# Optimization experiments

Hardware: AMD Instinct MI355X
Metric: run time of the kernel (lower is better)

The kernel has to match this reference:

```python
import jax, jax.numpy as jnp
import numpy as np

NORM_EPS = 1e-5
NUM_HEAD = 16
DIM_HEAD = 32
DIM_HIDDEN = 512
DIM_POS = 2
N, S = 4, 8192


def setup_inputs() -> dict:
    key = jax.random.key(0)
    ks = jax.random.split(key, 16)
    d = DIM_HIDDEN
    inp = {
        "Q": jax.random.normal(ks[0], (N, S, d), jnp.float32),
        "K": jax.random.normal(ks[1], (N, S, d), jnp.float32),
        "V": jax.random.normal(ks[2], (N, S, d), jnp.float32),
        "position": jax.random.uniform(ks[3], (N, S, DIM_POS), jnp.float32),
        "W_Q": jax.random.normal(ks[4], (d, d), jnp.float32) * (1.0 / np.sqrt(d)),
        "W_K": jax.random.normal(ks[5], (d, d), jnp.float32) * (1.0 / np.sqrt(d)),
        "W_V": jax.random.normal(ks[6], (d, d), jnp.float32) * (1.0 / np.sqrt(d)),
        "b_Q": jnp.zeros((d,), jnp.float32),
        "b_K": jnp.zeros((d,), jnp.float32),
        "b_V": jnp.zeros((d,), jnp.float32),
        "ln_w_K": jnp.ones((NUM_HEAD, DIM_HEAD), jnp.float32),
        "ln_b_K": jnp.zeros((NUM_HEAD, DIM_HEAD), jnp.float32),
        "ln_w_V": jnp.ones((NUM_HEAD, DIM_HEAD), jnp.float32),
        "ln_b_V": jnp.zeros((NUM_HEAD, DIM_HEAD), jnp.float32),
        # torch Linear(dim_hidden + dim_position*num_head, dim_hidden): weight [out, in]
        "fc_W": jax.random.normal(ks[7], (d, d + DIM_POS * NUM_HEAD), jnp.float32) * (1.0 / np.sqrt(d + DIM_POS * NUM_HEAD)),
        "fc_b": jnp.zeros((d,), jnp.float32),
    }
    return inp


def _proj_heads(x, W, b):
    # [N,S,D] @ [D,D] + [D] -> [N,H,S,Dh]
    n, s, d = x.shape
    y = x @ W + b
    return y.reshape(n, s, NUM_HEAD, DIM_HEAD).transpose(0, 2, 1, 3)


def _ln(x, w, b):
    # per-head layernorm over last dim; w,b: [H,Dh] broadcast as [1,H,1,Dh]
    mu = jnp.mean(x, axis=-1, keepdims=True)
    var = jnp.mean((x - mu) ** 2, axis=-1, keepdims=True)
    xn = (x - mu) * jax.lax.rsqrt(var + NORM_EPS)
    return xn * w[None, :, None, :] + b[None, :, None, :]


def reference(Q, K, V, position, W_Q, W_K, W_V, b_Q, b_K, b_V,
              ln_w_K, ln_b_K, ln_w_V, ln_b_V, fc_W, fc_b):
    n, s, d = Q.shape
    q = _proj_heads(Q, W_Q, b_Q)                    # [N,H,S,Dh]
    k = _ln(_proj_heads(K, W_K, b_K), ln_w_K, ln_b_K)
    v = _ln(_proj_heads(V, W_V, b_V), ln_w_V, ln_b_V)
    pos = jnp.broadcast_to(position[:, None, :, :], (n, NUM_HEAD, s, DIM_POS))
    q = jnp.concatenate([pos, q], axis=-1)          # [N,H,S,P+Dh]
    k = jnp.concatenate([pos, k], axis=-1)
    v = jnp.concatenate([pos, v], axis=-1)
    # Galerkin linear attention: Q @ (K^T V / seqlen), no softmax
    ktv = jnp.einsum('nhsd,nhse->nhde', k, v) / s   # [N,H,P+Dh,P+Dh]
    x = jnp.einsum('nhsd,nhde->nhse', q, ktv)       # [N,H,S,P+Dh]
    x = x.transpose(0, 2, 1, 3).reshape(n, s, NUM_HEAD * (DIM_POS + DIM_HEAD))
    return x @ fc_W.T + fc_b
```

## Files before the change

### kernel.cpp

```cpp
#include <hip/hip_runtime.h>
#include <hip/hip_bf16.h>

typedef short short8 __attribute__((ext_vector_type(8)));
typedef float f32x4 __attribute__((ext_vector_type(4)));
typedef unsigned int uint4v __attribute__((ext_vector_type(4)));

__device__ __forceinline__ short f2bf(float f) {
  unsigned u = __builtin_bit_cast(unsigned, f);
  u += 0x7fffu + ((u >> 16) & 1u);
  return (short)(u >> 16);
}
__device__ __forceinline__ float bf2f(short s) {
  unsigned u = ((unsigned)(unsigned short)s) << 16;
  return __builtin_bit_cast(float, u);
}
__device__ __forceinline__ unsigned pk2(float a, float b) {
  __hip_bfloat162 h = __float22bfloat162_rn(float2{a, b});
  unsigned u;
  __builtin_memcpy(&u, &h, 4);
  return u;
}
__device__ __forceinline__ void gl_lds16(const void* g, void* l) {
  __builtin_amdgcn_global_load_lds(
      (const __attribute__((address_space(1))) unsigned int*)g,
      (__attribute__((address_space(3))) unsigned int*)l, 16, 0, 0);
}

__global__ __launch_bounds__(256) void wt_kernel(
    const float* __restrict__ WK, const float* __restrict__ WV,
    short* __restrict__ Wt)
{
  const int z = blockIdx.z;
  const float* W = (z == 0) ? WK : WV;
  short* o = Wt + (size_t)z * 512 * 512;
  __shared__ short t[64][65];
  const int k0 = blockIdx.y * 64, n0 = blockIdx.x * 64;
  const int c = threadIdx.x & 63, rb = threadIdx.x >> 6;
#pragma unroll
  for (int p = 0; p < 16; ++p) {
    const int kk = p * 4 + rb;
    t[kk][c] = f2bf(W[(size_t)(k0 + kk) * 512 + n0 + c]);
  }
  __syncthreads();
#pragma unroll
  for (int p = 0; p < 16; ++p) {
    const int nn = p * 4 + rb;
    o[(size_t)(n0 + nn) * 512 + k0 + c] = t[c][nn];
  }
}

__global__ __launch_bounds__(512) void proj_kernel(
    const float* __restrict__ Kin, const float* __restrict__ Vin,
    const short* __restrict__ Wt,
    const float* __restrict__ bK, const float* __restrict__ bV,
    short* __restrict__ kp, short* __restrict__ vp)
{
  const int phys = blockIdx.x;
  const int log_ = (phys & 7) * 64 + (phys >> 3);
  const int z = log_ >> 8;
  const int rem = log_ & 255;
  const int row0 = (rem >> 1) * 256;
  const int col0 = (rem & 1) * 256;

  const float* X    = (z == 0) ? Kin : Vin;
  const float* bias = (z == 0) ? bK  : bV;
  const short* Wz   = Wt + (size_t)z * 512 * 512;
  short* dst        = (z == 0) ? kp : vp;

  __shared__ short a_lds[2][256 * 32];
  __shared__ short b_lds[2][256 * 32];

  const int tid = threadIdx.x;
  const int lane = tid & 63, wv = tid >> 6;
  const int wr = wv >> 2, wc = wv & 3;
  const int fr = lane & 15, fg = lane >> 4;

  f32x4 acc[8][4];
#pragma unroll
  for (int i = 0; i < 8; ++i)
#pragma unroll
    for (int j = 0; j < 4; ++j) acc[i][j] = (f32x4){0.f, 0.f, 0.f, 0.f};

  const int ar = tid >> 1;
  const int ak = (tid & 1) * 16;
  const int bl8 = lane * 8;

  {
#pragma unroll
    for (int i = 0; i < 2; ++i) {
      const int nb = i * 128 + wv * 16;
      gl_lds16(Wz + (size_t)(col0 + nb + (lane >> 2)) * 512 + (lane & 3) * 8,
               &b_lds[0][nb * 32 + bl8]);
    }
    const f32x4* ap = (const f32x4*)(X + (size_t)(row0 + ar) * 512 + ak);
    f32x4 f0 = ap[0], f1 = ap[1], f2 = ap[2], f3 = ap[3];
    uint4v s0, s1;
    s0[0] = pk2(f0[0], f0[1]); s0[1] = pk2(f0[2], f0[3]);
    s0[2] = pk2(f1[0], f1[1]); s0[3] = pk2(f1[2], f1[3]);
    s1[0] = pk2(f2[0], f2[1]); s1[1] = pk2(f2[2], f2[3]);
    s1[2] = pk2(f3[0], f3[1]); s1[3] = pk2(f3[2], f3[3]);
    *(uint4v*)&a_lds[0][ar * 32 + ak] = s0;
    *(uint4v*)&a_lds[0][ar * 32 + ak + 8] = s1;
  }
  __syncthreads();

  for (int t = 0; t < 16; ++t) {
    const int cur = t & 1;
    const bool pf = (t < 15);
    f32x4 p0, p1, p2, p3;
    if (pf) {
      const int k1 = (t + 1) * 32;
      short* bn = b_lds[cur ^ 1];
#pragma unroll
      for (int i = 0; i < 2; ++i) {
        const int nb = i * 128 + wv * 16;
        gl_lds16(Wz + (size_t)(col0 + nb + (lane >> 2)) * 512 + k1 + (lane & 3) * 8,
                 &bn[nb * 32 + bl8]);
      }
      const f32x4* ap = (const f32x4*)(X + (size_t)(row0 + ar) * 512 + k1 + ak);
      p0 = ap[0]; p1 = ap[1]; p2 = ap[2]; p3 = ap[3];
    }

    const short* acur = a_lds[cur];
    const short* bcur = b_lds[cur];
    short8 af[8], bfr[4];
#pragma unroll
    for (int mi = 0; mi < 8; ++mi)
      af[mi] = *(const short8*)&acur[(wr * 128 + mi * 16 + fr) * 32 + fg * 8];
#pragma unroll
    for (int ni = 0; ni < 4; ++ni)
      bfr[ni] = *(const short8*)&bcur[(wc * 64 + ni * 16 + fr) * 32 + fg * 8];
#pragma unroll
    for (int mi = 0; mi < 8; ++mi)
#pragma unroll
      for (int ni = 0; ni < 4; ++ni)
        acc[mi][ni] = __builtin_amdgcn_mfma_f32_16x16x32_bf16(af[mi], bfr[ni], acc[mi][ni], 0, 0, 0);

    if (pf) {
      short* an = a_lds[cur ^ 1];
      uint4v s0, s1;
      s0[0] = pk2(p0[0], p0[1]); s0[1] = pk2(p0[2], p0[3]);
      s0[2] = pk2(p1[0], p1[1]); s0[3] = pk2(p1[2], p1[3]);
      s1[0] = pk2(p2[0], p2[1]); s1[1] = pk2(p2[2], p2[3]);
      s1[2] = pk2(p3[0], p3[1]); s1[3] = pk2(p3[2], p3[3]);
      *(uint4v*)&an[ar * 32 + ak] = s0;
      *(uint4v*)&an[ar * 32 + ak + 8] = s1;
    }
    __syncthreads();
  }

#pragma unroll
  for (int ni = 0; ni < 4; ++ni) {
    const int gc = col0 + wc * 64 + ni * 16 + fr;
    const float bv = bias[gc];
#pragma unroll
    for (int mi = 0; mi < 8; ++mi) {
#pragma unroll
      for (int r = 0; r < 4; ++r) {
        const int gr = row0 + wr * 128 + mi * 16 + fg * 4 + r;
        dst[(size_t)gr * 512 + gc] = f2bf(acc[mi][ni][r] + bv);
      }
    }
  }
}

#define SC 256
#define TP 264

__global__ __launch_bounds__(256) void ktv_kernel(
    const short* __restrict__ kp, const short* __restrict__ vp,
    const float* __restrict__ pos,
    const float* __restrict__ lnwK, const float* __restrict__ lnbK,
    const float* __restrict__ lnwV, const float* __restrict__ lnbV,
    float* __restrict__ ktv)
{
  const int nh = blockIdx.y;
  const int n = nh >> 4, h = nh & 15;
  const int s0 = blockIdx.x * SC;
  const int tid = threadIdx.x;

  __shared__ short klds[48 * TP];
  __shared__ short vlds[48 * TP];
  __shared__ float lw[2][32], lb[2][32];

  if (tid < 32) {
    lw[0][tid] = lnwK[h * 32 + tid]; lb[0][tid] = lnbK[h * 32 + tid];
    lw[1][tid] = lnwV[h * 32 + tid]; lb[1][tid] = lnbV[h * 32 + tid];
  }
  __syncthreads();

  const size_t rowix = (size_t)n * 8192 + (s0 + tid);
  {
    const short8* src = (const short8*)(kp + rowix * 512 + h * 32);
    short8 r0 = src[0], r1 = src[1], r2 = src[2], r3 = src[3];
// ... 48 lines not shown
    for (int i = 0; i < 3; ++i) acc[i] = (f32x4){0.f, 0.f, 0.f, 0.f};
    for (int kk = 0; kk < SC; kk += 32) {
      short8 a = *(const short8*)&klds[(wv * 16 + fr) * TP + kk + fg * 8];
#pragma unroll
      for (int ni = 0; ni < 3; ++ni) {
        short8 b = *(const short8*)&vlds[(ni * 16 + fr) * TP + kk + fg * 8];
        acc[ni] = __builtin_amdgcn_mfma_f32_16x16x32_bf16(a, b, acc[ni], 0, 0, 0);
      }
    }
#pragma unroll
    for (int ni = 0; ni < 3; ++ni) {
      const int ei = ni * 16 + fr;
      if (ei < 34) {
        const int er = (ei < 32) ? ei + 2 : ei - 32;
#pragma unroll
        for (int r = 0; r < 4; ++r) {
          const int di = wv * 16 + fg * 4 + r;
          if (di < 34) {
            const int dr = (di < 32) ? di + 2 : di - 32;
            atomicAdd(&ktv[((size_t)nh * 34 + dr) * 34 + er], acc[ni][r]);
          }
        }
      }
    }
  }
}

__global__ __launch_bounds__(256) void sbuild_kernel(
    const float* __restrict__ ktv, const float* __restrict__ fcW,
    const float* __restrict__ bQ, float* __restrict__ St, float* __restrict__ Pp3)
{
  const int nh = blockIdx.x;
  const int n = nh >> 4, h = nh & 15;
  __shared__ float g[34 * 34];
  __shared__ float bq[32];
  for (int i = threadIdx.x; i < 34 * 34; i += 256)
    g[i] = ktv[(size_t)nh * 34 * 34 + i] * (1.f / 8192.f);
  if (threadIdx.x < 32) bq[threadIdx.x] = bQ[h * 32 + threadIdx.x];
  __syncthreads();

  for (int o = threadIdx.x; o < 512; o += 256) {
    float wcol[34];
#pragma unroll
    for (int e = 0; e < 34; ++e) wcol[e] = fcW[(size_t)o * 544 + h * 34 + e];
    float p0 = 0.f, p1 = 0.f;
#pragma unroll
    for (int e = 0; e < 34; ++e) { p0 += g[e] * wcol[e]; p1 += g[34 + e] * wcol[e]; }
    float rv = 0.f;
    float* srow = St + ((size_t)n * 512 + o) * 512 + h * 32;
#pragma unroll
    for (int j = 0; j < 32; ++j) {
      float s = 0.f;
#pragma unroll
      for (int e = 0; e < 34; ++e) s += g[(j + 2) * 34 + e] * wcol[e];
      srow[j] = s;
      rv += bq[j] * s;
    }
    atomicAdd(&Pp3[((size_t)n * 3 + 0) * 512 + o], p0);
    atomicAdd(&Pp3[((size_t)n * 3 + 1) * 512 + o], p1);
    atomicAdd(&Pp3[((size_t)n * 3 + 2) * 512 + o], rv);
  }
}

__global__ __launch_bounds__(256) void cbuild_kernel(
    const float* __restrict__ St, const float* __restrict__ WQ,
    short* __restrict__ Ct)
{
  const int n = blockIdx.z;
  const int row0 = blockIdx.y * 128;
  const int col0 = blockIdx.x * 128;
  const float* A = St + (size_t)n * 512 * 512;
  const float* B = WQ;

  __shared__ short a_lds[128 * 32];
  __shared__ short b_lds[128 * 32];

  const int tid = threadIdx.x;
  const int lane = tid & 63, wv = tid >> 6;
  const int wr = wv >> 1, wc = wv & 1;
  const int fr = lane & 15, fg = lane >> 4;
  const int ar = tid >> 1, ak = (tid & 1) * 16;

  f32x4 acc[4][4];
#pragma unroll
  for (int i = 0; i < 4; ++i)
#pragma unroll
    for (int j = 0; j < 4; ++j) acc[i][j] = (f32x4){0.f, 0.f, 0.f, 0.f};

  for (int k0 = 0; k0 < 512; k0 += 32) {
    __syncthreads();
    {
      const f32x4* ap = (const f32x4*)(A + (size_t)(row0 + ar) * 512 + k0 + ak);
      f32x4 f0 = ap[0], f1 = ap[1], f2 = ap[2], f3 = ap[3];
      uint4v s0, s1;
      s0[0] = pk2(f0[0], f0[1]); s0[1] = pk2(f0[2], f0[3]);
      s0[2] = pk2(f1[0], f1[1]); s0[3] = pk2(f1[2], f1[3]);
      s1[0] = pk2(f2[0], f2[1]); s1[1] = pk2(f2[2], f2[3]);
      s1[2] = pk2(f3[0], f3[1]); s1[3] = pk2(f3[2], f3[3]);
      *(uint4v*)&a_lds[ar * 32 + ak] = s0;
      *(uint4v*)&a_lds[ar * 32 + ak + 8] = s1;
      const f32x4* bp = (const f32x4*)(B + (size_t)(col0 + ar) * 512 + k0 + ak);
      f32x4 g0 = bp[0], g1 = bp[1], g2 = bp[2], g3 = bp[3];
      s0[0] = pk2(g0[0], g0[1]); s0[1] = pk2(g0[2], g0[3]);
      s0[2] = pk2(g1[0], g1[1]); s0[3] = pk2(g1[2], g1[3]);
      s1[0] = pk2(g2[0], g2[1]); s1[1] = pk2(g2[2], g2[3]);
      s1[2] = pk2(g3[0], g3[1]); s1[3] = pk2(g3[2], g3[3]);
      *(uint4v*)&b_lds[ar * 32 + ak] = s0;
      *(uint4v*)&b_lds[ar * 32 + ak + 8] = s1;
    }
    __syncthreads();

    short8 af[4], bfr[4];
#pragma unroll
    for (int mi = 0; mi < 4; ++mi)
      af[mi] = *(const short8*)&a_lds[(wr * 64 + mi * 16 + fr) * 32 + fg * 8];
#pragma unroll
    for (int ni = 0; ni < 4; ++ni)
      bfr[ni] = *(const short8*)&b_lds[(wc * 64 + ni * 16 + fr) * 32 + fg * 8];
#pragma unroll
    for (int mi = 0; mi < 4; ++mi)
#pragma unroll
      for (int ni = 0; ni < 4; ++ni)
        acc[mi][ni] = __builtin_amdgcn_mfma_f32_16x16x32_bf16(af[mi], bfr[ni], acc[mi][ni], 0, 0, 0);
  }

#pragma unroll
  for (int ni = 0; ni < 4; ++ni) {
    const int gc = col0 + wc * 64 + ni * 16 + fr;
#pragma unroll
    for (int mi = 0; mi < 4; ++mi)
#pragma unroll
      for (int r = 0; r < 4; ++r) {
        const int gr = row0 + wr * 64 + mi * 16 + fg * 4 + r;
        Ct[((size_t)n * 512 + gr) * 512 + gc] = f2bf(acc[mi][ni][r]);
      }
  }
}

__global__ __launch_bounds__(512) void fuse_kernel(
    const float* __restrict__ Q, const short* __restrict__ Ct,
    const float* __restrict__ pos, const float* __restrict__ Pp3,
    const float* __restrict__ fcb, float* __restrict__ out)
{
  const int phys = blockIdx.x;
  const int log_ = (phys & 7) * 32 + (phys >> 3);
  const int n = log_ >> 6;
  const int rem = log_ & 63;
  const int row0 = (rem >> 1) * 256;
  const int col0 = (rem & 1) * 256;

  const float* X = Q + (size_t)n * 8192 * 512;
  const short* B = Ct + (size_t)n * 512 * 512;

  __shared__ short a_lds[2][256 * 32];
  __shared__ short b_lds[2][256 * 32];

  const int tid = threadIdx.x;
  const int lane = tid & 63, wv = tid >> 6;
  const int wr = wv >> 2, wc = wv & 3;
  const int fr = lane & 15, fg = lane >> 4;

  f32x4 acc[8][4];
#pragma unroll
  for (int i = 0; i < 8; ++i)
#pragma unroll
    for (int j = 0; j < 4; ++j) acc[i][j] = (f32x4){0.f, 0.f, 0.f, 0.f};

  const int ar = tid >> 1;
  const int ak = (tid & 1) * 16;
  const int bl8 = lane * 8;

  {
#pragma unroll
    for (int i = 0; i < 2; ++i) {
      const int nb = i * 128 + wv * 16;
      gl_lds16(B + (size_t)(col0 + nb + (lane >> 2)) * 512 + (lane & 3) * 8,
               &b_lds[0][nb * 32 + bl8]);
    }
    const f32x4* ap = (const f32x4*)(X + (size_t)(row0 + ar) * 512 + ak);
    f32x4 f0 = ap[0], f1 = ap[1], f2 = ap[2], f3 = ap[3];
    uint4v s0, s1;
    s0[0] = pk2(f0[0], f0[1]); s0[1] = pk2(f0[2], f0[3]);
    s0[2] = pk2(f1[0], f1[1]); s0[3] = pk2(f1[2], f1[3]);
    s1[0] = pk2(f2[0], f2[1]); s1[1] = pk2(f2[2], f2[3]);
    s1[2] = pk2(f3[0], f3[1]); s1[3] = pk2(f3[2], f3[3]);
    *(uint4v*)&a_lds[0][ar * 32 + ak] = s0;
    *(uint4v*)&a_lds[0][ar * 32 + ak + 8] = s1;
  }
  __syncthreads();

  for (int t = 0; t < 16; ++t) {
    const int cur = t & 1;
    const bool pf = (t < 15);
    f32x4 p0, p1, p2, p3;
    if (pf) {
      const int k1 = (t + 1) * 32;
      short* bn = b_lds[cur ^ 1];
#pragma unroll
      for (int i = 0; i < 2; ++i) {
        const int nb = i * 128 + wv * 16;
        gl_lds16(B + (size_t)(col0 + nb + (lane >> 2)) * 512 + k1 + (lane & 3) * 8,
                 &bn[nb * 32 + bl8]);
      }
      const f32x4* ap = (const f32x4*)(X + (size_t)(row0 + ar) * 512 + k1 + ak);
      p0 = ap[0]; p1 = ap[1]; p2 = ap[2]; p3 = ap[3];
    }

    const short* acur = a_lds[cur];
    const short* bcur = b_lds[cur];
    short8 af[8], bfr[4];
#pragma unroll
    for (int mi = 0; mi < 8; ++mi)
      af[mi] = *(const short8*)&acur[(wr * 128 + mi * 16 + fr) * 32 + fg * 8];
#pragma unroll
    for (int ni = 0; ni < 4; ++ni)
      bfr[ni] = *(const short8*)&bcur[(wc * 64 + ni * 16 + fr) * 32 + fg * 8];
#pragma unroll
    for (int mi = 0; mi < 8; ++mi)
#pragma unroll
      for (int ni = 0; ni < 4; ++ni)
        acc[mi][ni] = __builtin_amdgcn_mfma_f32_16x16x32_bf16(af[mi], bfr[ni], acc[mi][ni], 0, 0, 0);

    if (pf) {
      short* an = a_lds[cur ^ 1];
      uint4v s0, s1;
      s0[0] = pk2(p0[0], p0[1]); s0[1] = pk2(p0[2], p0[3]);
      s0[2] = pk2(p1[0], p1[1]); s0[3] = pk2(p1[2], p1[3]);
      s1[0] = pk2(p2[0], p2[1]); s1[1] = pk2(p2[2], p2[3]);
      s1[2] = pk2(p3[0], p3[1]); s1[3] = pk2(p3[2], p3[3]);
      *(uint4v*)&an[ar * 32 + ak] = s0;
      *(uint4v*)&an[ar * 32 + ak + 8] = s1;
    }
    __syncthreads();
  }

  float pp0[4], pp1[4], rv[4];
#pragma unroll
  for (int ni = 0; ni < 4; ++ni) {
    const int gc = col0 + wc * 64 + ni * 16 + fr;
    pp0[ni] = Pp3[((size_t)n * 3 + 0) * 512 + gc];
    pp1[ni] = Pp3[((size_t)n * 3 + 1) * 512 + gc];
    rv[ni]  = Pp3[((size_t)n * 3 + 2) * 512 + gc] + fcb[gc];
  }
#pragma unroll
  for (int mi = 0; mi < 8; ++mi) {
#pragma unroll
    for (int r = 0; r < 4; ++r) {
      const int gr = row0 + wr * 128 + mi * 16 + fg * 4 + r;
      const float* pr = pos + ((size_t)n * 8192 + gr) * 2;
      const float q0 = pr[0], q1 = pr[1];
#pragma unroll
      for (int ni = 0; ni < 4; ++ni) {
        const int gc = col0 + wc * 64 + ni * 16 + fr;
        out[((size_t)n * 8192 + gr) * 512 + gc] =
            acc[mi][ni][r] + pp0[ni] * q0 + pp1[ni] * q1 + rv[ni];
      }
    }
  }
}

extern "C" void kernel_launch(void* const* d_in, const int* in_sizes, int n_in,
                              void* d_out, int out_size, void* d_ws, size_t ws_size,
                              hipStream_t stream) {
  const float* Q    = (const float*)d_in[0];
  const float* Kin  = (const float*)d_in[1];
  const float* Vin  = (const float*)d_in[2];
  const float* pos  = (const float*)d_in[3];
  const float* WQ   = (const float*)d_in[4];
  const float* WK   = (const float*)d_in[5];
  const float* WV   = (const float*)d_in[6];
  const float* bQ   = (const float*)d_in[7];
  const float* bK   = (const float*)d_in[8];
  const float* bV   = (const float*)d_in[9];
  const float* lnwK = (const float*)d_in[10];
  const float* lnbK = (const float*)d_in[11];
  const float* lnwV = (const float*)d_in[12];
  const float* lnbV = (const float*)d_in[13];
  const float* fcW  = (const float*)d_in[14];
  const float* fcb  = (const float*)d_in[15];

  char* ws = (char*)d_ws;
  const size_t KP_B  = (size_t)4 * 8192 * 512 * 2;
  const size_t KTV_B = (size_t)64 * 34 * 34 * 4;
  const size_t ST_B  = (size_t)4 * 512 * 512 * 4;
  const size_t CT_B  = (size_t)4 * 512 * 512 * 2;
  const size_t WT_B  = (size_t)2 * 512 * 512 * 2;
  const size_t PP_B  = (size_t)4 * 3 * 512 * 4;
  short* kp  = (short*)ws;
  short* vp  = (short*)(ws + KP_B);
  float* ktv = (float*)(ws + 2 * KP_B);
  float* St  = (float*)(ws + 2 * KP_B + KTV_B);
  short* Ct  = (short*)(ws + 2 * KP_B + KTV_B + ST_B);
  short* Wt  = (short*)(ws + 2 * KP_B + KTV_B + ST_B + CT_B);
  float* Pp3 = (float*)(ws + 2 * KP_B + KTV_B + ST_B + CT_B + WT_B);

  (void)hipMemsetAsync(ktv, 0, KTV_B, stream);
  (void)hipMemsetAsync(Pp3, 0, PP_B, stream);
  hipLaunchKernelGGL(wt_kernel, dim3(8, 8, 2), dim3(256), 0, stream, WK, WV, Wt);
  hipLaunchKernelGGL(proj_kernel, dim3(512), dim3(512), 0, stream,
                     Kin, Vin, Wt, bK, bV, kp, vp);
  hipLaunchKernelGGL(ktv_kernel, dim3(32, 64), dim3(256), 0, stream,
                     kp, vp, pos, lnwK, lnbK, lnwV, lnbV, ktv);
  hipLaunchKernelGGL(sbuild_kernel, dim3(64), dim3(256), 0, stream,
                     ktv, fcW, bQ, St, Pp3);
  hipLaunchKernelGGL(cbuild_kernel, dim3(4, 4, 4), dim3(256), 0, stream,
                     St, WQ, Ct);
  hipLaunchKernelGGL(fuse_kernel, dim3(256), dim3(512), 0, stream,
                     Q, Ct, pos, Pp3, fcb, (float*)d_out);
}
```

Before: 231.7 us.

## Deepen K tile to 64 with swizzled LDS and manual waitcnt pipelining in GEMMs

Both projection and fused output GEMM kernels now load 64-wide K tiles into XOR-swizzled LDS buffers. This halves loop iterations and barriers and aims to remove LDS bank conflicts on fragment reads. Synchronisation is replaced with explicit vmcnt/lgkmcnt waits, a single raw barrier, and elevated priority around MFMA bursts. The change doubles LDS use per block, which may limit occupancy despite the added launch-bounds hint.

```diff
diff --git a/kernel.cpp b/kernel.cpp
--- a/kernel.cpp
+++ b/kernel.cpp
@@ -49,7 +49,7 @@
   }
 }
 
-__global__ __launch_bounds__(512) void proj_kernel(
+__global__ __launch_bounds__(512, 2) void proj_kernel(
     const float* __restrict__ Kin, const float* __restrict__ Vin,
     const short* __restrict__ Wt,
     const float* __restrict__ bK, const float* __restrict__ bV,
@@ -67,13 +67,25 @@
   const short* Wz   = Wt + (size_t)z * 512 * 512;
   short* dst        = (z == 0) ? kp : vp;
 
-  __shared__ short a_lds[2][256 * 32];
-  __shared__ short b_lds[2][256 * 32];
+  __shared__ short a_lds[2][256 * 64];
+  __shared__ short b_lds[2][256 * 64];
 
   const int tid = threadIdx.x;
   const int lane = tid & 63, wv = tid >> 6;
   const int wr = wv >> 2, wc = wv & 3;
   const int fr = lane & 15, fg = lane >> 4;
+  const int sx = fr & 7;
+
+  const int arow = tid >> 1, aseg = tid & 1;
+  const float* abase = X + (size_t)(row0 + arow) * 512 + aseg * 32;
+  int awoff[4];
+#pragma unroll
+  for (int m = 0; m < 4; ++m)
+    awoff[m] = arow * 64 + (((aseg * 4 + m) ^ (arow & 7)) * 8);
+
+  const int brbase = col0 + wv * 32 + (lane >> 3);
+  const int bxor = ((lane & 7) ^ (lane >> 3)) * 8;
+  const int bldsbase = (wv * 32) * 64;
 
   f32x4 acc[8][4];
 #pragma unroll
@@ -81,72 +93,73 @@
 #pragma unroll
     for (int j = 0; j < 4; ++j) acc[i][j] = (f32x4){0.f, 0.f, 0.f, 0.f};
 
-  const int ar = tid >> 1;
-  const int ak = (tid & 1) * 16;
-  const int bl8 = lane * 8;
+  f32x4 pA[8];
 
   {
 #pragma unroll
-    for (int i = 0; i < 2; ++i) {
-      const int nb = i * 128 + wv * 16;
-      gl_lds16(Wz + (size_t)(col0 + nb + (lane >> 2)) * 512 + (lane & 3) * 8,
-               &b_lds[0][nb * 32 + bl8]);
-    }
-    const f32x4* ap = (const f32x4*)(X + (size_t)(row0 + ar) * 512 + ak);
-    f32x4 f0 = ap[0], f1 = ap[1], f2 = ap[2], f3 = ap[3];
-    uint4v s0, s1;
-    s0[0] = pk2(f0[0], f0[1]); s0[1] = pk2(f0[2], f0[3]);
-    s0[2] = pk2(f1[0], f1[1]); s0[3] = pk2(f1[2], f1[3]);
-    s1[0] = pk2(f2[0], f2[1]); s1[1] = pk2(f2[2], f2[3]);
-    s1[2] = pk2(f3[0], f3[1]); s1[3] = pk2(f3[2], f3[3]);
-    *(uint4v*)&a_lds[0][ar * 32 + ak] = s0;
-    *(uint4v*)&a_lds[0][ar * 32 + ak + 8] = s1;
-  }
-  __syncthreads();
-
-  for (int t = 0; t < 16; ++t) {
-    const int cur = t & 1;
-    const bool pf = (t < 15);
-    f32x4 p0, p1, p2, p3;
-    if (pf) {
-      const int k1 = (t + 1) * 32;
-      short* bn = b_lds[cur ^ 1];
-#pragma unroll
-      for (int i = 0; i < 2; ++i) {
-        const int nb = i * 128 + wv * 16;
-        gl_lds16(Wz + (size_t)(col0 + nb + (lane >> 2)) * 512 + k1 + (lane & 3) * 8,
-                 &bn[nb * 32 + bl8]);
-      }
-      const f32x4* ap = (const f32x4*)(X + (size_t)(row0 + ar) * 512 + k1 + ak);
-      p0 = ap[0]; p1 = ap[1]; p2 = ap[2]; p3 = ap[3];
-    }
-
-    const short* acur = a_lds[cur];
-    const short* bcur = b_lds[cur];
-    short8 af[8], bfr[4];
-#pragma unroll
-    for (int mi = 0; mi < 8; ++mi)
-      af[mi] = *(const short8*)&acur[(wr * 128 + mi * 16 + fr) * 32 + fg * 8];
-#pragma unroll
-    for (int ni = 0; ni < 4; ++ni)
-      bfr[ni] = *(const short8*)&bcur[(wc * 64 + ni * 16 + fr) * 32 + fg * 8];
-#pragma unroll
-    for (int mi = 0; mi < 8; ++mi)
+    for (int j = 0; j < 8; ++j) pA[j] = *(const f32x4*)(abase + j * 4);
+#pragma unroll
+    for (int i = 0; i < 4; ++i)
+      gl_lds16(Wz + (size_t)(brbase + i * 8) * 512 + bxor,
+               &b_lds[0][bldsbase + i * 8 * 64]);
+#pragma unroll
+    for (int m = 0; m < 4; ++m) {
+      uint4v s;
+      s[0] = pk2(pA[2*m][0], pA[2*m][1]);     s[1] = pk2(pA[2*m][2], pA[2*m][3]);
+      s[2] = pk2(pA[2*m+1][0], pA[2*m+1][1]); s[3] = pk2(pA[2*m+1][2], pA[2*m+1][3]);
+      *(uint4v*)&a_lds[0][awoff[m]] = s;
+    }
+  }
+
+  for (int t = 0; t < 8; ++t) {
+    if (t < 7) {
+      const float* ap = abase + (t + 1) * 64;
+#pragma unroll
+      for (int j = 0; j < 8; ++j) pA[j] = *(const f32x4*)(ap + j * 4);
+      asm volatile("s_waitcnt vmcnt(8) lgkmcnt(0)" ::: "memory");
+    } else {
+      asm volatile("s_waitcnt vmcnt(0) lgkmcnt(0)" ::: "memory");
+    }
+    __builtin_amdgcn_s_barrier();
+    __builtin_amdgcn_sched_barrier(0);
+    if (t < 7) {
+      short* bn = &b_lds[(t + 1) & 1][0];
+      const int k1 = (t + 1) * 64;
+#pragma unroll
+      for (int i = 0; i < 4; ++i)
+        gl_lds16(Wz + (size_t)(brbase + i * 8) * 512 + k1 + bxor,
+                 bn + bldsbase + i * 8 * 64);
+    }
+    const short* ac = &a_lds[t & 1][0];
+    const short* bc = &b_lds[t & 1][0];
+#pragma unroll
+    for (int kk = 0; kk < 2; ++kk) {
+      const int so = ((kk * 4 + fg) ^ sx) * 8;
+      short8 af[8], bfv[4];
 #pragma unroll
       for (int ni = 0; ni < 4; ++ni)
-        acc[mi][ni] = __builtin_amdgcn_mfma_f32_16x16x32_bf16(af[mi], bfr[ni], acc[mi][ni], 0, 0, 0);
-
-    if (pf) {
-      short* an = a_lds[cur ^ 1];
-      uint4v s0, s1;
-      s0[0] = pk2(p0[0], p0[1]); s0[1] = pk2(p0[2], p0[3]);
-      s0[2] = pk2(p1[0], p1[1]); s0[3] = pk2(p1[2], p1[3]);
-      s1[0] = pk2(p2[0], p2[1]); s1[1] = pk2(p2[2], p2[3]);
-      s1[2] = pk2(p3[0], p3[1]); s1[3] = pk2(p3[2], p3[3]);
-      *(uint4v*)&an[ar * 32 + ak] = s0;
-      *(uint4v*)&an[ar * 32 + ak + 8] = s1;
-    }
-    __syncthreads();
+        bfv[ni] = *(const short8*)&bc[(wc * 64 + ni * 16 + fr) * 64 + so];
+#pragma unroll
+      for (int mi = 0; mi < 8; ++mi)
+        af[mi] = *(const short8*)&ac[(wr * 128 + mi * 16 + fr) * 64 + so];
+      __builtin_amdgcn_s_setprio(1);
+#pragma unroll
+      for (int mi = 0; mi < 8; ++mi)
+#pragma unroll
+        for (int ni = 0; ni < 4; ++ni)
+          acc[mi][ni] = __builtin_amdgcn_mfma_f32_16x16x32_bf16(af[mi], bfv[ni], acc[mi][ni], 0, 0, 0);
+      __builtin_amdgcn_s_setprio(0);
+    }
+    if (t < 7) {
+      short* an = &a_lds[(t + 1) & 1][0];
+#pragma unroll
+      for (int m = 0; m < 4; ++m) {
+        uint4v s;
+        s[0] = pk2(pA[2*m][0], pA[2*m][1]);     s[1] = pk2(pA[2*m][2], pA[2*m][3]);
+        s[2] = pk2(pA[2*m+1][0], pA[2*m+1][1]); s[3] = pk2(pA[2*m+1][2], pA[2*m+1][3]);
+        *(uint4v*)&an[awoff[m]] = s;
+      }
+    }
   }
 
 #pragma unroll
@@ -379,7 +392,7 @@
   }
 }
 
-__global__ __launch_bounds__(512) void fuse_kernel(
+__global__ __launch_bounds__(512, 2) void fuse_kernel(
     const float* __restrict__ Q, const short* __restrict__ Ct,
     const float* __restrict__ pos, const float* __restrict__ Pp3,
     const float* __restrict__ fcb, float* __restrict__ out)
@@ -392,15 +405,27 @@
   const int col0 = (rem & 1) * 256;
 
   const float* X = Q + (size_t)n * 8192 * 512;
-  const short* B = Ct + (size_t)n * 512 * 512;
-
-  __shared__ short a_lds[2][256 * 32];
-  __shared__ short b_lds[2][256 * 32];
+  const short* Bz = Ct + (size_t)n * 512 * 512;
+
+  __shared__ short a_lds[2][256 * 64];
+  __shared__ short b_lds[2][256 * 64];
 
   const int tid = threadIdx.x;
   const int lane = tid & 63, wv = tid >> 6;
   const int wr = wv >> 2, wc = wv & 3;
   const int fr = lane & 15, fg = lane >> 4;
+  const int sx = fr & 7;
+
+  const int arow = tid >> 1, aseg = tid & 1;
+  const float* abase = X + (size_t)(row0 + arow) * 512 + aseg * 32;
+  int awoff[4];
+#pragma unroll
+  for (int m = 0; m < 4; ++m)
+    awoff[m] = arow * 64 + (((aseg * 4 + m) ^ (arow & 7)) * 8);
+
+  const int brbase = col0 + wv * 32 + (lane >> 3);
+  const int bxor = ((lane & 7) ^ (lane >> 3)) * 8;
+  const int bldsbase = (wv * 32) * 64;
 
   f32x4 acc[8][4];
 #pragma unroll
@@ -408,72 +433,73 @@
 #pragma unroll
     for (int j = 0; j < 4; ++j) acc[i][j] = (f32x4){0.f, 0.f, 0.f, 0.f};
 
-  const int ar = tid >> 1;
-  const int ak = (tid & 1) * 16;
-  const int bl8 = lane * 8;
+  f32x4 pA[8];
 
   {
 #pragma unroll
-    for (int i = 0; i < 2; ++i) {
-      const int nb = i * 128 + wv * 16;
-      gl_lds16(B + (size_t)(col0 + nb + (lane >> 2)) * 512 + (lane & 3) * 8,
-               &b_lds[0][nb * 32 + bl8]);
-    }
-    const f32x4* ap = (const f32x4*)(X + (size_t)(row0 + ar) * 512 + ak);
-    f32x4 f0 = ap[0], f1 = ap[1], f2 = ap[2], f3 = ap[3];
-    uint4v s0, s1;
-    s0[0] = pk2(f0[0], f0[1]); s0[1] = pk2(f0[2], f0[3]);
-    s0[2] = pk2(f1[0], f1[1]); s0[3] = pk2(f1[2], f1[3]);
-    s1[0] = pk2(f2[0], f2[1]); s1[1] = pk2(f2[2], f2[3]);
-    s1[2] = pk2(f3[0], f3[1]); s1[3] = pk2(f3[2], f3[3]);
-    *(uint4v*)&a_lds[0][ar * 32 + ak] = s0;
-    *(uint4v*)&a_lds[0][ar * 32 + ak + 8] = s1;
-  }
-  __syncthreads();
-
-  for (int t = 0; t < 16; ++t) {
-    const int cur = t & 1;
-    const bool pf = (t < 15);
-    f32x4 p0, p1, p2, p3;
-    if (pf) {
-      const int k1 = (t + 1) * 32;
-      short* bn = b_lds[cur ^ 1];
-#pragma unroll
-      for (int i = 0; i < 2; ++i) {
-        const int nb = i * 128 + wv * 16;
-        gl_lds16(B + (size_t)(col0 + nb + (lane >> 2)) * 512 + k1 + (lane & 3) * 8,
-                 &bn[nb * 32 + bl8]);
-      }
-      const f32x4* ap = (const f32x4*)(X + (size_t)(row0 + ar) * 512 + k1 + ak);
-      p0 = ap[0]; p1 = ap[1]; p2 = ap[2]; p3 = ap[3];
-    }
-
-    const short* acur = a_lds[cur];
-    const short* bcur = b_lds[cur];
-    short8 af[8], bfr[4];
-#pragma unroll
-    for (int mi = 0; mi < 8; ++mi)
-      af[mi] = *(const short8*)&acur[(wr * 128 + mi * 16 + fr) * 32 + fg * 8];
-#pragma unroll
-    for (int ni = 0; ni < 4; ++ni)
-      bfr[ni] = *(const short8*)&bcur[(wc * 64 + ni * 16 + fr) * 32 + fg * 8];
-#pragma unroll
-    for (int mi = 0; mi < 8; ++mi)
+    for (int j = 0; j < 8; ++j) pA[j] = *(const f32x4*)(abase + j * 4);
+#pragma unroll
+    for (int i = 0; i < 4; ++i)
+      gl_lds16(Bz + (size_t)(brbase + i * 8) * 512 + bxor,
+               &b_lds[0][bldsbase + i * 8 * 64]);
+#pragma unroll
+    for (int m = 0; m < 4; ++m) {
+      uint4v s;
+      s[0] = pk2(pA[2*m][0], pA[2*m][1]);     s[1] = pk2(pA[2*m][2], pA[2*m][3]);
+      s[2] = pk2(pA[2*m+1][0], pA[2*m+1][1]); s[3] = pk2(pA[2*m+1][2], pA[2*m+1][3]);
+      *(uint4v*)&a_lds[0][awoff[m]] = s;
+    }
+  }
+
+  for (int t = 0; t < 8; ++t) {
+    if (t < 7) {
+      const float* ap = abase + (t + 1) * 64;
+#pragma unroll
+      for (int j = 0; j < 8; ++j) pA[j] = *(const f32x4*)(ap + j * 4);
+      asm volatile("s_waitcnt vmcnt(8) lgkmcnt(0)" ::: "memory");
+    } else {
+      asm volatile("s_waitcnt vmcnt(0) lgkmcnt(0)" ::: "memory");
+    }
+    __builtin_amdgcn_s_barrier();
+    __builtin_amdgcn_sched_barrier(0);
+    if (t < 7) {
+      short* bn = &b_lds[(t + 1) & 1][0];
+      const int k1 = (t + 1) * 64;
+#pragma unroll
+      for (int i = 0; i < 4; ++i)
+        gl_lds16(Bz + (size_t)(brbase + i * 8) * 512 + k1 + bxor,
+                 bn + bldsbase + i * 8 * 64);
+    }
+    const short* ac = &a_lds[t & 1][0];
+    const short* bc = &b_lds[t & 1][0];
+#pragma unroll
+    for (int kk = 0; kk < 2; ++kk) {
+      const int so = ((kk * 4 + fg) ^ sx) * 8;
+      short8 af[8], bfv[4];
 #pragma unroll
       for (int ni = 0; ni < 4; ++ni)
-        acc[mi][ni] = __builtin_amdgcn_mfma_f32_16x16x32_bf16(af[mi], bfr[ni], acc[mi][ni], 0, 0, 0);
-
-    if (pf) {
-      short* an = a_lds[cur ^ 1];
-      uint4v s0, s1;
-      s0[0] = pk2(p0[0], p0[1]); s0[1] = pk2(p0[2], p0[3]);
-      s0[2] = pk2(p1[0], p1[1]); s0[3] = pk2(p1[2], p1[3]);
-      s1[0] = pk2(p2[0], p2[1]); s1[1] = pk2(p2[2], p2[3]);
-      s1[2] = pk2(p3[0], p3[1]); s1[3] = pk2(p3[2], p3[3]);
-      *(uint4v*)&an[ar * 32 + ak] = s0;
-      *(uint4v*)&an[ar * 32 + ak + 8] = s1;
-    }
-    __syncthreads();
+        bfv[ni] = *(const short8*)&bc[(wc * 64 + ni * 16 + fr) * 64 + so];
+#pragma unroll
+      for (int mi = 0; mi < 8; ++mi)
+        af[mi] = *(const short8*)&ac[(wr * 128 + mi * 16 + fr) * 64 + so];
+      __builtin_amdgcn_s_setprio(1);
+#pragma unroll
+      for (int mi = 0; mi < 8; ++mi)
+#pragma unroll
+        for (int ni = 0; ni < 4; ++ni)
+          acc[mi][ni] = __builtin_amdgcn_mfma_f32_16x16x32_bf16(af[mi], bfv[ni], acc[mi][ni], 0, 0, 0);
+      __builtin_amdgcn_s_setprio(0);
+    }
+    if (t < 7) {
+      short* an = &a_lds[(t + 1) & 1][0];
+#pragma unroll
+      for (int m = 0; m < 4; ++m) {
+        uint4v s;
+        s[0] = pk2(pA[2*m][0], pA[2*m][1]);     s[1] = pk2(pA[2*m][2], pA[2*m][3]);
+        s[2] = pk2(pA[2*m+1][0], pA[2*m+1][1]); s[3] = pk2(pA[2*m+1][2], pA[2*m+1][3]);
+        *(uint4v*)&an[awoff[m]] = s;
+      }
+    }
   }
 
   float pp0[4], pp1[4], rv[4];
```

After: 223.4 us. -3.6%, faster.

## Keep full B panel resident in LDS and stream A tiles in persistent GEMMs

Applied to the files above, without the earlier changes.

The projection and fuse GEMMs are restructured so each 256-thread block loads a whole 128x512 bf16 weight panel into LDS once, using an XOR swizzle. It then loops over many 128-row A tiles with a register-prefetched, double-buffered A pipeline, swizzled fragment reads and raised MFMA priority. This removes the repeated B reloads of the old 256x256 tiles and cuts barrier work per tile, at the cost of a large LDS footprint (about 144KB) and one block per CU. The sbuild kernel is also split four ways across the j dimension to use more blocks.

```diff
diff --git a/kernel.cpp b/kernel.cpp
--- a/kernel.cpp
+++ b/kernel.cpp
@@ -49,117 +49,132 @@
   }
 }
 
-__global__ __launch_bounds__(512) void proj_kernel(
+#define LDA(S, A0, A1, A2, A3) do { \
+    const int mt_ = (S) >> 4, tt_ = (S) & 15; \
+    const f32x4* ap_ = (const f32x4*)(abase + (size_t)(mt_ * 128 + ar) * 512 + tt_ * 32); \
+    A0 = ap_[0]; A1 = ap_[1]; A2 = ap_[2]; A3 = ap_[3]; } while (0)
+
+#define CVW(A0, A1, A2, A3, WB) do { \
+    uint4v s_; \
+    s_[0] = pk2(A0[0], A0[1]); s_[1] = pk2(A0[2], A0[3]); \
+    s_[2] = pk2(A1[0], A1[1]); s_[3] = pk2(A1[2], A1[3]); \
+    *(uint4v*)&(WB)[aw0] = s_; \
+    s_[0] = pk2(A2[0], A2[1]); s_[1] = pk2(A2[2], A2[3]); \
+    s_[2] = pk2(A3[0], A3[1]); s_[3] = pk2(A3[2], A3[3]); \
+    *(uint4v*)&(WB)[aw1] = s_; } while (0)
+
+#define FRAGS(AB, TT) do { \
+    const int ko_ = ((TT) >> 1) * 64; \
+    const int kb_ = (((TT) & 1) << 2) | fg; \
+    for (int i_ = 0; i_ < 4; ++i_) { \
+      bfv[i_] = *(const short8*)&b_lds[boff[i_] + ko_ + ((kb_ ^ bx[i_]) * 8)]; \
+      af[i_] = *(const short8*)&(AB)[aoff[i_]]; \
+    } } while (0)
+
+#define MFMA16() do { \
+    __builtin_amdgcn_s_setprio(1); \
+    for (int mi_ = 0; mi_ < 4; ++mi_) \
+      for (int ni_ = 0; ni_ < 4; ++ni_) \
+        acc[mi_][ni_] = __builtin_amdgcn_mfma_f32_16x16x32_bf16(af[mi_], bfv[ni_], acc[mi_][ni_], 0, 0, 0); \
+    __builtin_amdgcn_s_setprio(0); } while (0)
+
+#define BARRIER() do { \
+    asm volatile("s_waitcnt lgkmcnt(0)" ::: "memory"); \
+    __builtin_amdgcn_s_barrier(); } while (0)
+
+__global__ __launch_bounds__(256) void proj_kernel(
     const float* __restrict__ Kin, const float* __restrict__ Vin,
     const short* __restrict__ Wt,
     const float* __restrict__ bK, const float* __restrict__ bV,
     short* __restrict__ kp, short* __restrict__ vp)
 {
   const int phys = blockIdx.x;
-  const int log_ = (phys & 7) * 64 + (phys >> 3);
-  const int z = log_ >> 8;
-  const int rem = log_ & 255;
-  const int row0 = (rem >> 1) * 256;
-  const int col0 = (rem & 1) * 256;
-
-  const float* X    = (z == 0) ? Kin : Vin;
-  const float* bias = (z == 0) ? bK  : bV;
-  const short* Wz   = Wt + (size_t)z * 512 * 512;
-  short* dst        = (z == 0) ? kp : vp;
-
-  __shared__ short a_lds[2][256 * 32];
-  __shared__ short b_lds[2][256 * 32];
+  const int log_ = (phys & 7) * 32 + (phys >> 3);
+  const int z = log_ >> 7;
+  const int col0 = ((log_ >> 5) & 3) * 128;
+  const int m0 = (log_ & 31) * 1024;
+
+  const float* X = z ? Vin : Kin;
+  const short* Bsrc = Wt + (size_t)z * 512 * 512;
+  const float* bias = z ? bV : bK;
+  short* dst = z ? vp : kp;
+
+  __shared__ short b_lds[128 * 512];
+  __shared__ short a_lds[2][128 * 32];
 
   const int tid = threadIdx.x;
   const int lane = tid & 63, wv = tid >> 6;
-  const int wr = wv >> 2, wc = wv & 3;
+  const int wr = wv >> 1, wc = wv & 1;
   const int fr = lane & 15, fg = lane >> 4;
 
-  f32x4 acc[8][4];
-#pragma unroll
-  for (int i = 0; i < 8; ++i)
+#pragma unroll
+  for (int it = 0; it < 32; ++it) {
+    const int row = wv * 32 + it;
+    const int srck = (lane >> 3) * 64 + (((lane & 7) ^ (row & 7)) * 8);
+    gl_lds16(Bsrc + (size_t)(col0 + row) * 512 + srck, &b_lds[row * 512 + lane * 8]);
+  }
+
+  const int ar = tid >> 1, ah = tid & 1;
+  const int am = (ar & 3) ^ ((ar >> 2) & 3);
+  const int aw0 = ar * 32 + (((2 * ah) ^ am) & 3) * 8;
+  const int aw1 = ar * 32 + (((2 * ah + 1) ^ am) & 3) * 8;
+  const float* abase = X + (size_t)m0 * 512 + ah * 16;
+
+  int aoff[4], boff[4], bx[4];
+#pragma unroll
+  for (int i = 0; i < 4; ++i) {
+    const int ra = wr * 64 + i * 16 + fr;
+    aoff[i] = ra * 32 + (((fg ^ (ra & 3) ^ ((ra >> 2) & 3)) & 3) * 8);
+    const int rb = wc * 64 + i * 16 + fr;
+    boff[i] = rb * 512;
+    bx[i] = rb & 7;
+  }
+
+  f32x4 acc[4][4];
+#pragma unroll
+  for (int i = 0; i < 4; ++i)
 #pragma unroll
     for (int j = 0; j < 4; ++j) acc[i][j] = (f32x4){0.f, 0.f, 0.f, 0.f};
 
-  const int ar = tid >> 1;
-  const int ak = (tid & 1) * 16;
-  const int bl8 = lane * 8;
-
-  {
-#pragma unroll
-    for (int i = 0; i < 2; ++i) {
-      const int nb = i * 128 + wv * 16;
-      gl_lds16(Wz + (size_t)(col0 + nb + (lane >> 2)) * 512 + (lane & 3) * 8,
-               &b_lds[0][nb * 32 + bl8]);
-    }
-    const f32x4* ap = (const f32x4*)(X + (size_t)(row0 + ar) * 512 + ak);
-    f32x4 f0 = ap[0], f1 = ap[1], f2 = ap[2], f3 = ap[3];
-    uint4v s0, s1;
-    s0[0] = pk2(f0[0], f0[1]); s0[1] = pk2(f0[2], f0[3]);
-    s0[2] = pk2(f1[0], f1[1]); s0[3] = pk2(f1[2], f1[3]);
-    s1[0] = pk2(f2[0], f2[1]); s1[1] = pk2(f2[2], f2[3]);
-    s1[2] = pk2(f3[0], f3[1]); s1[3] = pk2(f3[2], f3[3]);
-    *(uint4v*)&a_lds[0][ar * 32 + ak] = s0;
-    *(uint4v*)&a_lds[0][ar * 32 + ak + 8] = s1;
-  }
-  __syncthreads();
-
-  for (int t = 0; t < 16; ++t) {
-    const int cur = t & 1;
-    const bool pf = (t < 15);
-    f32x4 p0, p1, p2, p3;
-    if (pf) {
-      const int k1 = (t + 1) * 32;
-      short* bn = b_lds[cur ^ 1];
-#pragma unroll
-      for (int i = 0; i < 2; ++i) {
-        const int nb = i * 128 + wv * 16;
-        gl_lds16(Wz + (size_t)(col0 + nb + (lane >> 2)) * 512 + k1 + (lane & 3) * 8,
-                 &bn[nb * 32 + bl8]);
+  f32x4 pe0, pe1, pe2, pe3, po0, po1, po2, po3;
+  short8 af[4], bfv[4];
+  const int NSTEP = 128;
+
+  LDA(0, pe0, pe1, pe2, pe3);
+  LDA(1, po0, po1, po2, po3);
+  CVW(pe0, pe1, pe2, pe3, a_lds[0]);
+  asm volatile("s_waitcnt vmcnt(0) lgkmcnt(0)" ::: "memory");
+  __builtin_amdgcn_s_barrier();
+
+  for (int s = 0; s < NSTEP; s += 2) {
+    {
+      FRAGS(a_lds[0], s & 15);
+      if (s + 2 < NSTEP) LDA(s + 2, pe0, pe1, pe2, pe3);
+      MFMA16();
+      CVW(po0, po1, po2, po3, a_lds[1]);
+      BARRIER();
+    }
+    {
+      const int so = s + 1;
+      FRAGS(a_lds[1], so & 15);
+      if (so + 2 < NSTEP) LDA(so + 2, po0, po1, po2, po3);
+      MFMA16();
+      if (so + 1 < NSTEP) CVW(pe0, pe1, pe2, pe3, a_lds[0]);
+      if ((so & 15) == 15) {
+        const int mt = so >> 4;
+        for (int ni = 0; ni < 4; ++ni) {
+          const int gc = col0 + wc * 64 + ni * 16 + fr;
+          const float bv = bias[gc];
+          for (int mi = 0; mi < 4; ++mi)
+            for (int r = 0; r < 4; ++r) {
+              const int gr = m0 + mt * 128 + wr * 64 + mi * 16 + fg * 4 + r;
+              dst[(size_t)gr * 512 + gc] = f2bf(acc[mi][ni][r] + bv);
+            }
+        }
+        for (int i = 0; i < 4; ++i)
+          for (int j = 0; j < 4; ++j) acc[i][j] = (f32x4){0.f, 0.f, 0.f, 0.f};
       }
-      const f32x4* ap = (const f32x4*)(X + (size_t)(row0 + ar) * 512 + k1 + ak);
-      p0 = ap[0]; p1 = ap[1]; p2 = ap[2]; p3 = ap[3];
-    }
-
-    const short* acur = a_lds[cur];
-    const short* bcur = b_lds[cur];
-    short8 af[8], bfr[4];
-#pragma unroll
-    for (int mi = 0; mi < 8; ++mi)
-      af[mi] = *(const short8*)&acur[(wr * 128 + mi * 16 + fr) * 32 + fg * 8];
-#pragma unroll
-    for (int ni = 0; ni < 4; ++ni)
-      bfr[ni] = *(const short8*)&bcur[(wc * 64 + ni * 16 + fr) * 32 + fg * 8];
-#pragma unroll
-    for (int mi = 0; mi < 8; ++mi)
-#pragma unroll
-      for (int ni = 0; ni < 4; ++ni)
-        acc[mi][ni] = __builtin_amdgcn_mfma_f32_16x16x32_bf16(af[mi], bfr[ni], acc[mi][ni], 0, 0, 0);
-
-    if (pf) {
-      short* an = a_lds[cur ^ 1];
-      uint4v s0, s1;
-      s0[0] = pk2(p0[0], p0[1]); s0[1] = pk2(p0[2], p0[3]);
-      s0[2] = pk2(p1[0], p1[1]); s0[3] = pk2(p1[2], p1[3]);
-      s1[0] = pk2(p2[0], p2[1]); s1[1] = pk2(p2[2], p2[3]);
-      s1[2] = pk2(p3[0], p3[1]); s1[3] = pk2(p3[2], p3[3]);
-      *(uint4v*)&an[ar * 32 + ak] = s0;
-      *(uint4v*)&an[ar * 32 + ak + 8] = s1;
-    }
-    __syncthreads();
-  }
-
-#pragma unroll
-  for (int ni = 0; ni < 4; ++ni) {
-    const int gc = col0 + wc * 64 + ni * 16 + fr;
-    const float bv = bias[gc];
-#pragma unroll
-    for (int mi = 0; mi < 8; ++mi) {
-#pragma unroll
-      for (int r = 0; r < 4; ++r) {
-        const int gr = row0 + wr * 128 + mi * 16 + fg * 4 + r;
-        dst[(size_t)gr * 512 + gc] = f2bf(acc[mi][ni][r] + bv);
-      }
+      BARRIER();
     }
   }
 }
@@ -274,33 +289,37 @@
 {
   const int nh = blockIdx.x;
   const int n = nh >> 4, h = nh & 15;
+  const int jq = blockIdx.y;
   __shared__ float g[34 * 34];
-  __shared__ float bq[32];
+  __shared__ float bq8[8];
   for (int i = threadIdx.x; i < 34 * 34; i += 256)
     g[i] = ktv[(size_t)nh * 34 * 34 + i] * (1.f / 8192.f);
-  if (threadIdx.x < 32) bq[threadIdx.x] = bQ[h * 32 + threadIdx.x];
+  if (threadIdx.x < 8) bq8[threadIdx.x] = bQ[h * 32 + jq * 8 + threadIdx.x];
   __syncthreads();
 
   for (int o = threadIdx.x; o < 512; o += 256) {
     float wcol[34];
 #pragma unroll
     for (int e = 0; e < 34; ++e) wcol[e] = fcW[(size_t)o * 544 + h * 34 + e];
-    float p0 = 0.f, p1 = 0.f;
-#pragma unroll
-    for (int e = 0; e < 34; ++e) { p0 += g[e] * wcol[e]; p1 += g[34 + e] * wcol[e]; }
     float rv = 0.f;
-    float* srow = St + ((size_t)n * 512 + o) * 512 + h * 32;
-#pragma unroll
-    for (int j = 0; j < 32; ++j) {
+    float* srow = St + ((size_t)n * 512 + o) * 512 + h * 32 + jq * 8;
+#pragma unroll
+    for (int jj = 0; jj < 8; ++jj) {
+      const int j = jq * 8 + jj;
       float s = 0.f;
 #pragma unroll
       for (int e = 0; e < 34; ++e) s += g[(j + 2) * 34 + e] * wcol[e];
-      srow[j] = s;
-      rv += bq[j] * s;
-    }
-    atomicAdd(&Pp3[((size_t)n * 3 + 0) * 512 + o], p0);
-    atomicAdd(&Pp3[((size_t)n * 3 + 1) * 512 + o], p1);
+      srow[jj] = s;
+      rv += bq8[jj] * s;
+    }
     atomicAdd(&Pp3[((size_t)n * 3 + 2) * 512 + o], rv);
+    if (jq == 0) {
+      float p0 = 0.f, p1 = 0.f;
+#pragma unroll
+      for (int e = 0; e < 34; ++e) { p0 += g[e] * wcol[e]; p1 += g[34 + e] * wcol[e]; }
+      atomicAdd(&Pp3[((size_t)n * 3 + 0) * 512 + o], p0);
+      atomicAdd(&Pp3[((size_t)n * 3 + 1) * 512 + o], p1);
+    }
   }
 }
 
@@ -315,7 +334,7 @@
   const float* B = WQ;
 
   __shared__ short a_lds[128 * 32];
-  __shared__ short b_lds[128 * 32];
+  __shared__ short b_lds2[128 * 32];
 
   const int tid = threadIdx.x;
   const int lane = tid & 63, wv = tid >> 6;
@@ -347,8 +366,8 @@
       s0[2] = pk2(g1[0], g1[1]); s0[3] = pk2(g1[2], g1[3]);
       s1[0] = pk2(g2[0], g2[1]); s1[1] = pk2(g2[2], g2[3]);
       s1[2] = pk2(g3[0], g3[1]); s1[3] = pk2(g3[2], g3[3]);
-      *(uint4v*)&b_lds[ar * 32 + ak] = s0;
-      *(uint4v*)&b_lds[ar * 32 + ak + 8] = s1;
+      *(uint4v*)&b_lds2[ar * 32 + ak] = s0;
+      *(uint4v*)&b_lds2[ar * 32 + ak + 8] = s1;
     }
     __syncthreads();
 
@@ -358,7 +377,7 @@
       af[mi] = *(const short8*)&a_lds[(wr * 64 + mi * 16 + fr) * 32 + fg * 8];
 #pragma unroll
     for (int ni = 0; ni < 4; ++ni)
-      bfr[ni] = *(const short8*)&b_lds[(wc * 64 + ni * 16 + fr) * 32 + fg * 8];
+      bfr[ni] = *(const short8*)&b_lds2[(wc * 64 + ni * 16 + fr) * 32 + fg * 8];
 #pragma unroll
     for (int mi = 0; mi < 4; ++mi)
 #pragma unroll
@@ -379,7 +398,7 @@
   }
 }
 
-__global__ __launch_bounds__(512) void fuse_kernel(
+__global__ __launch_bounds__(256) void fuse_kernel(
     const float* __restrict__ Q, const short* __restrict__ Ct,
     const float* __restrict__ pos, const float* __restrict__ Pp3,
     const float* __restrict__ fcb, float* __restrict__ out)
@@ -387,93 +406,43 @@
   const int phys = blockIdx.x;
   const int log_ = (phys & 7) * 32 + (phys >> 3);
   const int n = log_ >> 6;
-  const int rem = log_ & 63;
-  const int row0 = (rem >> 1) * 256;
-  const int col0 = (rem & 1) * 256;
+  const int col0 = ((log_ >> 4) & 3) * 128;
+  const int m0 = (log_ & 15) * 512;
 
   const float* X = Q + (size_t)n * 8192 * 512;
-  const short* B = Ct + (size_t)n * 512 * 512;
-
-  __shared__ short a_lds[2][256 * 32];
-  __shared__ short b_lds[2][256 * 32];
+  const short* Bsrc = Ct + (size_t)n * 512 * 512;
+  float* dstf = out + (size_t)n * 8192 * 512;
+  const float* posn = pos + (size_t)n * 8192 * 2;
+
+  __shared__ short b_lds[128 * 512];
+  __shared__ short a_lds[2][128 * 32];
 
   const int tid = threadIdx.x;
   const int lane = tid & 63, wv = tid >> 6;
-  const int wr = wv >> 2, wc = wv & 3;
+  const int wr = wv >> 1, wc = wv & 1;
   const int fr = lane & 15, fg = lane >> 4;
 
-  f32x4 acc[8][4];
-#pragma unroll
-  for (int i = 0; i < 8; ++i)
-#pragma unroll
-    for (int j = 0; j < 4; ++j) acc[i][j] = (f32x4){0.f, 0.f, 0.f, 0.f};
-
-  const int ar = tid >> 1;
-  const int ak = (tid & 1) * 16;
-  const int bl8 = lane * 8;
-
-  {
-#pragma unroll
-    for (int i = 0; i < 2; ++i) {
-      const int nb = i * 128 + wv * 16;
-      gl_lds16(B + (size_t)(col0 + nb + (lane >> 2)) * 512 + (lane & 3) * 8,
-               &b_lds[0][nb * 32 + bl8]);
-    }
-    const f32x4* ap = (const f32x4*)(X + (size_t)(row0 + ar) * 512 + ak);
-    f32x4 f0 = ap[0], f1 = ap[1], f2 = ap[2], f3 = ap[3];
-    uint4v s0, s1;
-    s0[0] = pk2(f0[0], f0[1]); s0[1] = pk2(f0[2], f0[3]);
-    s0[2] = pk2(f1[0], f1[1]); s0[3] = pk2(f1[2], f1[3]);
-    s1[0] = pk2(f2[0], f2[1]); s1[1] = pk2(f2[2], f2[3]);
-    s1[2] = pk2(f3[0], f3[1]); s1[3] = pk2(f3[2], f3[3]);
-    *(uint4v*)&a_lds[0][ar * 32 + ak] = s0;
-    *(uint4v*)&a_lds[0][ar * 32 + ak + 8] = s1;
-  }
-  __syncthreads();
-
-  for (int t = 0; t < 16; ++t) {
-    const int cur = t & 1;
-    const bool pf = (t < 15);
-    f32x4 p0, p1, p2, p3;
-    if (pf) {
-      const int k1 = (t + 1) * 32;
-      short* bn = b_lds[cur ^ 1];
-#pragma unroll
-      for (int i = 0; i < 2; ++i) {
-        const int nb = i * 128 + wv * 16;
-        gl_lds16(B + (size_t)(col0 + nb + (lane >> 2)) * 512 + k1 + (lane & 3) * 8,
-                 &bn[nb * 32 + bl8]);
-      }
-      const f32x4* ap = (const f32x4*)(X + (size_t)(row0 + ar) * 512 + k1 + ak);
-      p0 = ap[0]; p1 = ap[1]; p2 = ap[2]; p3 = ap[3];
-    }
-
-    const short* acur = a_lds[cur];
-    const short* bcur = b_lds[cur];
-    short8 af[8], bfr[4];
-#pragma unroll
-    for (int mi = 0; mi < 8; ++mi)
-      af[mi] = *(const short8*)&acur[(wr * 128 + mi * 16 + fr) * 32 + fg * 8];
-#pragma unroll
-    for (int ni = 0; ni < 4; ++ni)
-      bfr[ni] = *(const short8*)&bcur[(wc * 64 + ni * 16 + fr) * 32 + fg * 8];
-#pragma unroll
-    for (int mi = 0; mi < 8; ++mi)
-#pragma unroll
-      for (int ni = 0; ni < 4; ++ni)
-        acc[mi][ni] = __builtin_amdgcn_mfma_f32_16x16x32_bf16(af[mi], bfr[ni], acc[mi][ni], 0, 0, 0);
-
-    if (pf) {
-      short* an = a_lds[cur ^ 1];
-      uint4v s0, s1;
-      s0[0] = pk2(p0[0], p0[1]); s0[1] = pk2(p0[2], p0[3]);
-      s0[2] = pk2(p1[0], p1[1]); s0[3] = pk2(p1[2], p1[3]);
-      s1[0] = pk2(p2[0], p2[1]); s1[1] = pk2(p2[2], p2[3]);
-      s1[2] = pk2(p3[0], p3[1]); s1[3] = pk2(p3[2], p3[3]);
-      *(uint4v*)&an[ar * 32 + ak] = s0;
-      *(uint4v*)&an[ar * 32 + ak + 8] = s1;
-    }
-    __syncthreads();
+#pragma unroll
+  for (int it = 0; it < 32; ++it) {
+    const int row = wv * 32 + it;
+    const int srck = (lane >> 3) * 64 + (((lane & 7) ^ (row & 7)) * 8);
+    gl_lds16(Bsrc + (size_t)(col0 + row) * 512 + srck, &b_lds[row * 512 + lane * 8]);
+  }
+
+  const int ar = tid >> 1, ah = tid & 1;
+  const int am = (ar & 3) ^ ((ar >> 2) & 3);
+  const int aw0 = ar * 32 + (((2 * ah) ^ am) & 3) * 8;
+  const int aw1 = ar * 32 + (((2 * ah + 1) ^ am) & 3) * 8;
+  const float* abase = X + (size_t)m0 * 512 + ah * 16;
+
+  int aoff[4], boff[4], bx[4];
+#pragma unroll
+  for (int i = 0; i < 4; ++i) {
+    const int ra = wr * 64 + i * 16 + fr;
+    aoff[i] = ra * 32 + (((fg ^ (ra & 3) ^ ((ra >> 2) & 3)) & 3) * 8);
+    const int rb = wc * 64 + i * 16 + fr;
+    boff[i] = rb * 512;
+    bx[i] = rb & 7;
   }
 
   float pp0[4], pp1[4], rv[4];
@@ -484,19 +453,54 @@
     pp1[ni] = Pp3[((size_t)n * 3 + 1) * 512 + gc];
     rv[ni]  = Pp3[((size_t)n * 3 + 2) * 512 + gc] + fcb[gc];
   }
-#pragma unroll
-  for (int mi = 0; mi < 8; ++mi) {
-#pragma unroll
-    for (int r = 0; r < 4; ++r) {
-      const int gr = row0 + wr * 128 + mi * 16 + fg * 4 + r;
-      const float* pr = pos + ((size_t)n * 8192 + gr) * 2;
-      const float q0 = pr[0], q1 = pr[1];
-#pragma unroll
-      for (int ni = 0; ni < 4; ++ni) {
-        const int gc = col0 + wc * 64 + ni * 16 + fr;
-        out[((size_t)n * 8192 + gr) * 512 + gc] =
-            acc[mi][ni][r] + pp0[ni] * q0 + pp1[ni] * q1 + rv[ni];
+
+  f32x4 acc[4][4];
+#pragma unroll
+  for (int i = 0; i < 4; ++i)
+#pragma unroll
+    for (int j = 0; j < 4; ++j) acc[i][j] = (f32x4){0.f, 0.f, 0.f, 0.f};
+
+  f32x4 pe0, pe1, pe2, pe3, po0, po1, po2, po3;
+  short8 af[4], bfv[4];
+  const int NSTEP = 64;
+
+  LDA(0, pe0, pe1, pe2, pe3);
+  LDA(1, po0, po1, po2, po3);
+  CVW(pe0, pe1, pe2, pe3, a_lds[0]);
+  asm volatile("s_waitcnt vmcnt(0) lgkmcnt(0)" ::: "memory");
+  __builtin_amdgcn_s_barrier();
+
+  for (int s = 0; s < NSTEP; s += 2) {
+    {
+      FRAGS(a_lds[0], s & 15);
+      if (s + 2 < NSTEP) LDA(s + 2, pe0, pe1, pe2, pe3);
+      MFMA16();
+      CVW(po0, po1, po2, po3, a_lds[1]);
+      BARRIER();
+    }
+    {
+      const int so = s + 1;
+      FRAGS(a_lds[1], so & 15);
+      if (so + 2 < NSTEP) LDA(so + 2, po0, po1, po2, po3);
+      MFMA16();
+      if (so + 1 < NSTEP) CVW(pe0, pe1, pe2, pe3, a_lds[0]);
+      if ((so & 15) == 15) {
+        const int mt = so >> 4;
+        for (int mi = 0; mi < 4; ++mi)
+          for (int r = 0; r < 4; ++r) {
+            const int gr = m0 + mt * 128 + wr * 64 + mi * 16 + fg * 4 + r;
+            const float q0 = posn[(size_t)gr * 2];
+            const float q1 = posn[(size_t)gr * 2 + 1];
+            for (int ni = 0; ni < 4; ++ni) {
+              const int gc = col0 + wc * 64 + ni * 16 + fr;
+              dstf[(size_t)gr * 512 + gc] =
+                  acc[mi][ni][r] + pp0[ni] * q0 + pp1[ni] * q1 + rv[ni];
+            }
+          }
+        for (int i = 0; i < 4; ++i)
+          for (int j = 0; j < 4; ++j) acc[i][j] = (f32x4){0.f, 0.f, 0.f, 0.f};
       }
+      BARRIER();
     }
   }
 }
@@ -539,14 +543,14 @@
   (void)hipMemsetAsync(ktv, 0, KTV_B, stream);
   (void)hipMemsetAsync(Pp3, 0, PP_B, stream);
   hipLaunchKernelGGL(wt_kernel, dim3(8, 8, 2), dim3(256), 0, stream, WK, WV, Wt);
-  hipLaunchKernelGGL(proj_kernel, dim3(512), dim3(512), 0, stream,
+  hipLaunchKernelGGL(proj_kernel, dim3(256), dim3(256), 0, stream,
                      Kin, Vin, Wt, bK, bV, kp, vp);
   hipLaunchKernelGGL(ktv_kernel, dim3(32, 64), dim3(256), 0, stream,
                      kp, vp, pos, lnwK, lnbK, lnwV, lnbV, ktv);
-  hipLaunchKernelGGL(sbuild_kernel, dim3(64), dim3(256), 0, stream,
+  hipLaunchKernelGGL(sbuild_kernel, dim3(64, 4), dim3(256), 0, stream,
                      ktv, fcW, bQ, St, Pp3);
   hipLaunchKernelGGL(cbuild_kernel, dim3(4, 4, 4), dim3(256), 0, stream,
                      St, WQ, Ct);
-  hipLaunchKernelGGL(fuse_kernel, dim3(256), dim3(512), 0, stream,
+  hipLaunchKernelGGL(fuse_kernel, dim3(256), dim3(256), 0, stream,
                      Q, Ct, pos, Pp3, fcb, (float*)d_out);
 }
```

Result: slower. 307.4 us (+32.7%).
